# Optimization experiments

Hardware: AMD Instinct MI355X
Metric: run time of the kernel (lower is better)

Reference implementation:

```python
import jax, jax.numpy as jnp
import numpy as np

N_NODES = 100000
N_EDGES = 1600000
D_IN = 128
D_OUT = 128


def setup_inputs() -> dict:
    key = jax.random.key(0)
    k1, k2, k3, k4, k5 = jax.random.split(key, 5)
    H = jax.random.normal(k1, (N_NODES, D_IN), dtype=jnp.float32)
    vals = jax.random.uniform(k2, (N_EDGES,), dtype=jnp.float32)
    W = jax.random.normal(k3, (D_OUT, D_IN), dtype=jnp.float32) * (1.0 / np.sqrt(D_IN))
    rows = jax.random.randint(k4, (N_EDGES,), 0, N_NODES, dtype=jnp.int32)
    cols = jax.random.randint(k5, (N_EDGES,), 0, N_NODES, dtype=jnp.int32)
    return {"H": H, "vals": vals, "W": W, "rows": rows, "cols": cols}


def reference(H, vals, W, rows, cols):
    # Single-rank: communicate_fgm is a no-op (X is zeros, no remote peers).
    # SpMM: out[i] = sum_e vals[e] * H[cols[e]] for edges with rows[e] == i
    msgs = vals[:, None] * H[cols]                      # [n_edges, d_in] irregular gather
    AH = jax.ops.segment_sum(msgs, rows, num_segments=N_NODES)  # [n_nodes, d_in]
    # Linear (no bias) + ReLU
    out = jax.nn.relu(AH @ W.T)                          # [n_nodes, d_out]
    return out
```

## Files before the change

kernel.cpp:

```cpp
#include <hip/hip_runtime.h>

#define N_NODES 100000
#define N_EDGES 1600000
#define D 128

#define NB 1563
#define SLOT 1280
#define CHUNK 2500
#define NBLK_BUCKET 640
#define NTILES 6250
#define CAPR 48

#define WB_OFF     0u
#define HWB_OFF    65536u
#define BCNT_OFF   25665536u
#define EPACK0_OFF 25673728u

typedef unsigned int uint;
typedef __attribute__((ext_vector_type(4))) float f32x4;
typedef __attribute__((ext_vector_type(8))) short bf16x8;

__device__ __forceinline__ unsigned short f2bf(float x) {
    uint u = __float_as_uint(x);
    uint r = u + 0x7fffu + ((u >> 16) & 1u);
    return (unsigned short)(r >> 16);
}

__device__ __forceinline__ void acc8(float acc[8], uint4 q, float v) {
    acc[0] = fmaf(v, __uint_as_float(q.x << 16),         acc[0]);
    acc[1] = fmaf(v, __uint_as_float(q.x & 0xffff0000u), acc[1]);
    acc[2] = fmaf(v, __uint_as_float(q.y << 16),         acc[2]);
    acc[3] = fmaf(v, __uint_as_float(q.y & 0xffff0000u), acc[3]);
    acc[4] = fmaf(v, __uint_as_float(q.z << 16),         acc[4]);
    acc[5] = fmaf(v, __uint_as_float(q.z & 0xffff0000u), acc[5]);
    acc[6] = fmaf(v, __uint_as_float(q.w << 16),         acc[6]);
    acc[7] = fmaf(v, __uint_as_float(q.w & 0xffff0000u), acc[7]);
}

__global__ void k_cast_zero(const float* __restrict__ W, unsigned short* __restrict__ Wb,
                            int* __restrict__ bcnt) {
    int b = blockIdx.x;
    if (b < 64) {
        int i = b * 256 + threadIdx.x;
        Wb[i] = f2bf(W[i]);
    } else {
        int j = (b - 64) * 256 + threadIdx.x;
        if (j < NB) bcnt[j] = 0;
    }
}

__global__ __launch_bounds__(256) void k_gemm_mfma(const float* __restrict__ H,
                                                   const unsigned short* __restrict__ Wb,
                                                   unsigned short* __restrict__ HWb) {
    const int wave = threadIdx.x >> 6;
    const int lane = threadIdx.x & 63;
    const int rowtile = blockIdx.x * 4 + wave;
    if (rowtile >= NTILES) return;
    const int rowbase = rowtile * 16;
    const int m    = lane & 15;
    const int quad = lane >> 4;

    f32x4 acc[8];
    #pragma unroll
    for (int nt = 0; nt < 8; ++nt) acc[nt] = (f32x4){0.f, 0.f, 0.f, 0.f};

    const float* hrow = H + (size_t)(rowbase + m) * D;

    #pragma unroll
    for (int ks = 0; ks < 4; ++ks) {
        const int k0 = ks * 32 + quad * 8;
        float4 a0 = *(const float4*)(hrow + k0);
        float4 a1 = *(const float4*)(hrow + k0 + 4);
        bf16x8 afr;
        afr[0] = (short)f2bf(a0.x); afr[1] = (short)f2bf(a0.y);
        afr[2] = (short)f2bf(a0.z); afr[3] = (short)f2bf(a0.w);
        afr[4] = (short)f2bf(a1.x); afr[5] = (short)f2bf(a1.y);
        afr[6] = (short)f2bf(a1.z); afr[7] = (short)f2bf(a1.w);
        #pragma unroll
        for (int nt = 0; nt < 8; ++nt) {
            bf16x8 bfr = *(const bf16x8*)(Wb + (size_t)(nt * 16 + m) * D + k0);
            acc[nt] = __builtin_amdgcn_mfma_f32_16x16x32_bf16(afr, bfr, acc[nt], 0, 0, 0);
        }
    }

    #pragma unroll
    for (int nt = 0; nt < 8; ++nt) {
        #pragma unroll
        for (int r = 0; r < 4; ++r) {
            int orow = rowbase + quad * 4 + r;
            HWb[(size_t)orow * D + nt * 16 + m] = f2bf(acc[nt][r]);
        }
    }
}

__global__ __launch_bounds__(256) void k_bucket(const int* __restrict__ rows,
                                                const int* __restrict__ cols,
                                                const float* __restrict__ vals,
                                                int* __restrict__ bcnt,
                                                int2* __restrict__ epack0) {
    __shared__ int hist[NB];
    __shared__ int cur[NB];
    const int tid = threadIdx.x;
    const int e0  = blockIdx.x * CHUNK;

    for (int b = tid; b < NB; b += 256) hist[b] = 0;
    __syncthreads();

    for (int i = tid; i < CHUNK; i += 256)
        atomicAdd(&hist[rows[e0 + i] >> 6], 1);
    __syncthreads();

    for (int b = tid; b < NB; b += 256) {
        int c = hist[b];
        int base = (c > 0) ? atomicAdd(&bcnt[b], c) : 0;
        cur[b] = b * SLOT + base;
    }
    __syncthreads();

    for (int i = tid; i < CHUNK; i += 256) {
        int r = rows[e0 + i];
        int p = atomicAdd(&cur[r >> 6], 1);
        epack0[p] = make_int2(((r & 63) << 17) | cols[e0 + i],
                              __float_as_int(vals[e0 + i]));
    }
}

__global__ __launch_bounds__(256) void k_spmm_half(const int* __restrict__ bcnt,
                                                   const int2* __restrict__ epack0,
                                                   const unsigned short* __restrict__ HWb,
                                                   float* __restrict__ out) {
    __shared__ int2 sE[32][CAPR + 1];
    __shared__ int  cnt[32];
    const int tid  = threadIdx.x;
    const int b    = blockIdx.x >> 1;
    const int half = blockIdx.x & 1;
    const int base = b * SLOT;
    const int n_e  = bcnt[b];

    if (tid < 32) cnt[tid] = 0;
    __syncthreads();

    for (int i = tid; i < n_e; i += 256) {
        int2 e  = epack0[base + i];
        int  lr = e.x >> 17;
        if ((lr >> 5) == half) {
            int l = lr & 31;
            int k = atomicAdd(&cnt[l], 1);
            if (k < CAPR) sE[l][k] = make_int2(e.x & 0x1FFFF, e.y);
        }
    }
    __syncthreads();

    const int lane  = tid & 15;
    const int group = tid >> 4;

    #pragma unroll
    for (int rr = 0; rr < 2; ++rr) {
        const int l   = group * 2 + rr;
        const int row = b * 64 + half * 32 + l;
        if (row >= N_NODES) continue;
        const int e_  = min(cnt[l], CAPR);

        float acc[8];
        #pragma unroll
        for (int c = 0; c < 8; ++c) acc[c] = 0.f;

        int j = 0;
        for (; j + 3 < e_; j += 4) {
            int2 e0 = sE[l][j],     e1 = sE[l][j + 1];
            int2 e2 = sE[l][j + 2], e3 = sE[l][j + 3];
            uint4 q0 = ((const uint4*)(HWb + (size_t)e0.x * D))[lane];
            uint4 q1 = ((const uint4*)(HWb + (size_t)e1.x * D))[lane];
            uint4 q2 = ((const uint4*)(HWb + (size_t)e2.x * D))[lane];
            uint4 q3 = ((const uint4*)(HWb + (size_t)e3.x * D))[lane];
            acc8(acc, q0, __int_as_float(e0.y));
            acc8(acc, q1, __int_as_float(e1.y));
            acc8(acc, q2, __int_as_float(e2.y));
            acc8(acc, q3, __int_as_float(e3.y));
        }
        for (; j < e_; ++j) {
            int2 e = sE[l][j];
            uint4 q = ((const uint4*)(HWb + (size_t)e.x * D))[lane];
            acc8(acc, q, __int_as_float(e.y));
        }

        float4 o0 = make_float4(fmaxf(acc[0], 0.f), fmaxf(acc[1], 0.f),
                                fmaxf(acc[2], 0.f), fmaxf(acc[3], 0.f));
        float4 o1 = make_float4(fmaxf(acc[4], 0.f), fmaxf(acc[5], 0.f),
                                fmaxf(acc[6], 0.f), fmaxf(acc[7], 0.f));
        ((float4*)out)[row * 32 + lane * 2]     = o0;
        ((float4*)out)[row * 32 + lane * 2 + 1] = o1;
    }
}

extern "C" void kernel_launch(void* const* d_in, const int* in_sizes, int n_in,
                              void* d_out, int out_size, void* d_ws, size_t ws_size,
                              hipStream_t stream) {
    const float* H    = (const float*)d_in[0];
    const float* vals = (const float*)d_in[1];
    const float* W    = (const float*)d_in[2];
    const int*   rows = (const int*)d_in[3];
    const int*   cols = (const int*)d_in[4];
    float* out = (float*)d_out;

    char* ws = (char*)d_ws;
    unsigned short* Wb     = (unsigned short*)(ws + WB_OFF);
    unsigned short* HWb    = (unsigned short*)(ws + HWB_OFF);
    int*            bcnt   = (int*)(ws + BCNT_OFF);
    int2*           epack0 = (int2*)(ws + EPACK0_OFF);

    k_cast_zero<<<64 + (NB + 255) / 256, 256, 0, stream>>>(W, Wb, bcnt);

    k_gemm_mfma<<<(NTILES + 3) / 4, 256, 0, stream>>>(H, Wb, HWb);

    k_bucket<<<NBLK_BUCKET, 256, 0, stream>>>(rows, cols, vals, bcnt, epack0);
    k_spmm_half<<<2 * NB, 256, 0, stream>>>(bcnt, epack0, HWb, out);
}
```

Before: 264.3 us.

## Split edge bucketing into two-level radix pass and merge SpMM halves

Replaces the single-pass bucketing by 64-row bucket with a two-level scatter: first into 512-row super-buckets, then each super-bucket is split into 8 sub-buckets. Scatter writes become more localized, and each block's histogram shrinks to fewer global atomics. The SpMM kernel now handles all 64 rows of a bucket in one 512-thread block rather than two half blocks, so each bucket's edge list is read once instead of twice. The cost is an extra kernel launch and an extra read and write of the edge list.

```diff
diff --git a/kernel.cpp b/kernel.cpp
--- a/kernel.cpp
+++ b/kernel.cpp
@@ -4,17 +4,21 @@
 #define N_EDGES 1600000
 #define D 128
 
+#define NSUP 196
+#define SLOTA 8960
+#define CHUNKA 3200
+#define NBLKA 500
 #define NB 1563
 #define SLOT 1280
-#define CHUNK 2500
-#define NBLK_BUCKET 640
 #define NTILES 6250
 #define CAPR 48
 
 #define WB_OFF     0u
 #define HWB_OFF    65536u
 #define BCNT_OFF   25665536u
-#define EPACK0_OFF 25673728u
+#define SCNTA_OFF  25673728u
+#define EPACKA_OFF 25677824u
+#define EPACK0_OFF 39727104u
 
 typedef unsigned int uint;
 typedef __attribute__((ext_vector_type(4))) float f32x4;
@@ -38,7 +42,7 @@
 }
 
 __global__ void k_cast_zero(const float* __restrict__ W, unsigned short* __restrict__ Wb,
-                            int* __restrict__ bcnt) {
+                            int* __restrict__ bcnt, int* __restrict__ scntA) {
     int b = blockIdx.x;
     if (b < 64) {
         int i = b * 256 + threadIdx.x;
@@ -46,6 +50,7 @@
     } else {
         int j = (b - 64) * 256 + threadIdx.x;
         if (j < NB) bcnt[j] = 0;
+        else if (j < NB + NSUP) scntA[j - NB] = 0;
     }
 }
 
@@ -93,61 +98,97 @@
     }
 }
 
-__global__ __launch_bounds__(256) void k_bucket(const int* __restrict__ rows,
-                                                const int* __restrict__ cols,
-                                                const float* __restrict__ vals,
-                                                int* __restrict__ bcnt,
-                                                int2* __restrict__ epack0) {
-    __shared__ int hist[NB];
-    __shared__ int cur[NB];
+__global__ __launch_bounds__(256) void k_bucket_super(const int* __restrict__ rows,
+                                                      const int* __restrict__ cols,
+                                                      const float* __restrict__ vals,
+                                                      int* __restrict__ scntA,
+                                                      int2* __restrict__ epackA) {
+    __shared__ int hist[NSUP];
+    __shared__ int cur[NSUP];
     const int tid = threadIdx.x;
-    const int e0  = blockIdx.x * CHUNK;
-
-    for (int b = tid; b < NB; b += 256) hist[b] = 0;
-    __syncthreads();
-
-    for (int i = tid; i < CHUNK; i += 256)
-        atomicAdd(&hist[rows[e0 + i] >> 6], 1);
-    __syncthreads();
-
-    for (int b = tid; b < NB; b += 256) {
-        int c = hist[b];
+    const int e0  = blockIdx.x * CHUNKA;
+
+    if (tid < NSUP) hist[tid] = 0;
+    __syncthreads();
+
+    for (int i = tid; i < CHUNKA; i += 256)
+        atomicAdd(&hist[rows[e0 + i] >> 9], 1);
+    __syncthreads();
+
+    if (tid < NSUP) {
+        int c = hist[tid];
+        int base = (c > 0) ? atomicAdd(&scntA[tid], c) : 0;
+        cur[tid] = tid * SLOTA + base;
+    }
+    __syncthreads();
+
+    for (int i = tid; i < CHUNKA; i += 256) {
+        int r = rows[e0 + i];
+        int s = r >> 9;
+        int p = atomicAdd(&cur[s], 1);
+        if (p < (s + 1) * SLOTA)
+            epackA[p] = make_int2(((r & 511) << 17) | cols[e0 + i],
+                                  __float_as_int(vals[e0 + i]));
+    }
+}
+
+__global__ __launch_bounds__(256) void k_bucket_sub(const int* __restrict__ scntA,
+                                                    const int2* __restrict__ epackA,
+                                                    int* __restrict__ bcnt,
+                                                    int2* __restrict__ epack0) {
+    __shared__ int hist8[8];
+    __shared__ int cur8[8];
+    const int tid = threadIdx.x;
+    const int s   = blockIdx.x >> 3;
+    const int q   = blockIdx.x & 7;
+    const int n   = min(scntA[s], SLOTA);
+    const int lo  = (n * q) >> 3;
+    const int hi  = (n * (q + 1)) >> 3;
+    const int2* src = epackA + (size_t)s * SLOTA;
+
+    if (tid < 8) hist8[tid] = 0;
+    __syncthreads();
+
+    for (int i = lo + tid; i < hi; i += 256)
+        atomicAdd(&hist8[(src[i].x >> 23) & 7], 1);
+    __syncthreads();
+
+    if (tid < 8) {
+        int c = hist8[tid];
+        int b = s * 8 + tid;
         int base = (c > 0) ? atomicAdd(&bcnt[b], c) : 0;
-        cur[b] = b * SLOT + base;
-    }
-    __syncthreads();
-
-    for (int i = tid; i < CHUNK; i += 256) {
-        int r = rows[e0 + i];
-        int p = atomicAdd(&cur[r >> 6], 1);
-        epack0[p] = make_int2(((r & 63) << 17) | cols[e0 + i],
-                              __float_as_int(vals[e0 + i]));
-    }
-}
-
-__global__ __launch_bounds__(256) void k_spmm_half(const int* __restrict__ bcnt,
-                                                   const int2* __restrict__ epack0,
-                                                   const unsigned short* __restrict__ HWb,
-                                                   float* __restrict__ out) {
-    __shared__ int2 sE[32][CAPR + 1];
-    __shared__ int  cnt[32];
+        cur8[tid] = b * SLOT + base;
+    }
+    __syncthreads();
+
+    for (int i = lo + tid; i < hi; i += 256) {
+        int2 e   = src[i];
+        int  sub = (e.x >> 23) & 7;
+        int  p   = atomicAdd(&cur8[sub], 1);
+        if (p < (s * 8 + sub + 1) * SLOT)
+            epack0[p] = make_int2(e.x & 0x7FFFFF, e.y);
+    }
+}
+
+__global__ __launch_bounds__(512) void k_spmm_b64(const int* __restrict__ bcnt,
+                                                  const int2* __restrict__ epack0,
+                                                  const unsigned short* __restrict__ HWb,
+                                                  float* __restrict__ out) {
+    __shared__ int2 sE[64][CAPR + 1];
+    __shared__ int  cnt[64];
     const int tid  = threadIdx.x;
-    const int b    = blockIdx.x >> 1;
-    const int half = blockIdx.x & 1;
+    const int b    = blockIdx.x;
     const int base = b * SLOT;
-    const int n_e  = bcnt[b];
-
-    if (tid < 32) cnt[tid] = 0;
-    __syncthreads();
-
-    for (int i = tid; i < n_e; i += 256) {
+    const int n_e  = min(bcnt[b], SLOT);
+
+    if (tid < 64) cnt[tid] = 0;
+    __syncthreads();
+
+    for (int i = tid; i < n_e; i += 512) {
         int2 e  = epack0[base + i];
         int  lr = e.x >> 17;
-        if ((lr >> 5) == half) {
-            int l = lr & 31;
-            int k = atomicAdd(&cnt[l], 1);
-            if (k < CAPR) sE[l][k] = make_int2(e.x & 0x1FFFF, e.y);
-        }
+        int  k  = atomicAdd(&cnt[lr], 1);
+        if (k < CAPR) sE[lr][k] = make_int2(e.x & 0x1FFFF, e.y);
     }
     __syncthreads();
 
@@ -157,7 +198,7 @@
     #pragma unroll
     for (int rr = 0; rr < 2; ++rr) {
         const int l   = group * 2 + rr;
-        const int row = b * 64 + half * 32 + l;
+        const int row = b * 64 + l;
         if (row >= N_NODES) continue;
         const int e_  = min(cnt[l], CAPR);
 
@@ -207,12 +248,16 @@
     unsigned short* Wb     = (unsigned short*)(ws + WB_OFF);
     unsigned short* HWb    = (unsigned short*)(ws + HWB_OFF);
     int*            bcnt   = (int*)(ws + BCNT_OFF);
+    int*            scntA  = (int*)(ws + SCNTA_OFF);
+    int2*           epackA = (int2*)(ws + EPACKA_OFF);
     int2*           epack0 = (int2*)(ws + EPACK0_OFF);
 
-    k_cast_zero<<<64 + (NB + 255) / 256, 256, 0, stream>>>(W, Wb, bcnt);
+    k_cast_zero<<<71, 256, 0, stream>>>(W, Wb, bcnt, scntA);
 
     k_gemm_mfma<<<(NTILES + 3) / 4, 256, 0, stream>>>(H, Wb, HWb);
 
-    k_bucket<<<NBLK_BUCKET, 256, 0, stream>>>(rows, cols, vals, bcnt, epack0);
-    k_spmm_half<<<2 * NB, 256, 0, stream>>>(bcnt, epack0, HWb, out);
-}
+    k_bucket_super<<<NBLKA, 256, 0, stream>>>(rows, cols, vals, scntA, epackA);
+    k_bucket_sub<<<NSUP * 8, 256, 0, stream>>>(scntA, epackA, bcnt, epack0);
+
+    k_spmm_b64<<<NB, 512, 0, stream>>>(bcnt, epack0, HWb, out);
+}
```

After: 251.9 us. 1.05x faster.
